# Kernel optimization log

Hardware: AMD Instinct MI355X
Metric: run time of the kernel (lower is better)

The kernel has to match this reference:

```python
import jax, jax.numpy as jnp
import numpy as np

N, DIM, K = 131072, 64, 1024


def setup_inputs() -> dict:
    key = jax.random.key(0)
    kx, ke = jax.random.split(key)
    x = jax.random.normal(kx, (N, DIM), dtype=jnp.float32)
    # codebook buffer, initialized like uniform(-1/K, 1/K) in the original
    scale = 1.0 / K
    embedding = jax.random.uniform(ke, (K, DIM), dtype=jnp.float32, minval=-scale, maxval=scale)
    return {"x": x, "embedding": embedding}


def reference(x, embedding):
    # squared euclidean distances in fp32 (matches compute_distances)
    x32 = x.astype(jnp.float32)
    e32 = embedding.astype(jnp.float32)
    distances = (
        jnp.sum(x32 * x32, axis=1, keepdims=True)
        + jnp.sum(e32 * e32, axis=1)
        - 2.0 * jnp.einsum("nd,kd->nk", x32, e32)
    )
    indices = jnp.argmin(distances, axis=1)          # (N,)
    quantized = embedding[indices]                    # (N, DIM) codebook gather
    # commitment loss: mse(stop_grad(quantized), x)
    commitment_loss = jnp.mean((jax.lax.stop_gradient(quantized) - x) ** 2)
    # straight-through estimator
    quantized_st = x + jax.lax.stop_gradient(quantized - x)
    return quantized_st, indices, commitment_loss
```

## Files before the change

kernel.cpp:

```cpp
#include <hip/hip_runtime.h>
#include <hip/hip_bf16.h>

#define N_ROWS 131072
#define DIM 64
#define K_CODES 1024
#define NTILES 64
#define MARGIN 4e-5f
#define LIST_CAP 65536

typedef short short8 __attribute__((ext_vector_type(8)));
typedef float f32x4 __attribute__((ext_vector_type(4)));

__device__ __forceinline__ unsigned short f2bf(float f) {
    unsigned u = __float_as_uint(f);
    return (unsigned short)((u + 0x7fffu + ((u >> 16) & 1u)) >> 16);
}
__device__ __forceinline__ float bf2f(unsigned short h) {
    return __uint_as_float(((unsigned)h) << 16);
}

__device__ __forceinline__ float np_sq64(const float* __restrict__ v) {
    float xx[DIM];
    #pragma unroll
    for (int d = 0; d < DIM; ++d) xx[d] = v[d] * v[d];
    float r[8];
    #pragma unroll
    for (int j = 0; j < 8; ++j) r[j] = xx[j];
    #pragma unroll
    for (int i = 8; i < DIM; i += 8)
        #pragma unroll
        for (int j = 0; j < 8; ++j) r[j] = r[j] + xx[i + j];
    return ((r[0]+r[1]) + (r[2]+r[3])) + ((r[4]+r[5]) + (r[6]+r[7]));
}

__device__ __forceinline__ float np_dot64(const float* __restrict__ xv,
                                          const float* __restrict__ ek) {
    float a0 = 0.f, a1 = 0.f, a2 = 0.f, a3 = 0.f;
    #pragma unroll
    for (int c = 0; c < DIM; c += 16)
        #pragma unroll
        for (int b = 12; b >= 0; b -= 4) {
            const int d = c + b;
            a0 = a0 + xv[d+0] * ek[d+0];
            a1 = a1 + xv[d+1] * ek[d+1];
            a2 = a2 + xv[d+2] * ek[d+2];
            a3 = a3 + xv[d+3] * ek[d+3];
        }
    return (a0 + a1) + (a2 + a3);
}


__global__ void vq_prep(const float* __restrict__ emb, float* __restrict__ esq,
                        unsigned short* __restrict__ wsB,
                        unsigned int* __restrict__ cnt, float* __restrict__ loss) {
#pragma clang fp contract(off)
    const int t = blockIdx.x * blockDim.x + threadIdx.x;
    if (t == 0) { *cnt = 0u; *loss = 0.f; }
    const int k = t >> 2, c = t & 3;
    if (k >= K_CODES) return;
    const float* e = emb + (size_t)k * DIM;

    if (c == 0) esq[k] = np_sq64(e);

    const int off = (c & 1) * 32, sel = c >> 1;
    unsigned short val[32];
    #pragma unroll
    for (int j = 0; j < 32; ++j) {
        float v = e[off + j];
        unsigned short h = f2bf(v);
        val[j] = sel ? f2bf(v - bf2f(h)) : h;
    }
    const int tile = k >> 4, n = k & 15;
    #pragma unroll
    for (int g = 0; g < 4; ++g) {
        short8 s;
        #pragma unroll
        for (int j = 0; j < 8; ++j) s[j] = (short)val[g*8 + j];
        *reinterpret_cast<short8*>(wsB + ((size_t)((tile*4 + c)*64 + g*16 + n)) * 8) = s;
    }
}

__global__ __launch_bounds__(256, 2) void vq_mfma(const float* __restrict__ x,
        const float* __restrict__ emb, const float* __restrict__ esq,
        const unsigned short* __restrict__ wsB, float* __restrict__ out,
        unsigned int* __restrict__ cnt, unsigned int* __restrict__ list,
        float* __restrict__ loss) {
#pragma clang fp contract(off)
    const int tid = threadIdx.x;
    const int lane = tid & 63;
    const int w = tid >> 6;
    const int g = lane >> 4, res = lane & 15;
    const int rowbase = blockIdx.x * 256 + w * 64;

    auto loadB = [&](short8* Bd, int ct) {
        const unsigned short* bp = wsB + ((size_t)(ct*4)*64 + lane) * 8;
        #pragma unroll
        for (int c = 0; c < 4; ++c)
            Bd[c] = *reinterpret_cast<const short8*>(bp + (size_t)c * 64 * 8);
    };

    short8 B0[4], B1[4], B2[4], B3[4];
    loadB(B0, 0); loadB(B1, 1); loadB(B2, 2); loadB(B3, 3);
    float e0 = esq[res], e1 = esq[16 + res];

    short8 Ah[4][2], Al[4][2];
    #pragma unroll
    for (int rg = 0; rg < 4; ++rg) {
        const float* xr = x + (size_t)(rowbase + rg*16 + res) * DIM;
        #pragma unroll
        for (int h = 0; h < 2; ++h) {
            float4 v0 = *reinterpret_cast<const float4*>(xr + h*32 + g*8);
            float4 v1 = *reinterpret_cast<const float4*>(xr + h*32 + g*8 + 4);
            float xv[8] = {v0.x, v0.y, v0.z, v0.w, v1.x, v1.y, v1.z, v1.w};
            short8 sh, sl;
            #pragma unroll
            for (int j = 0; j < 8; ++j) {
                unsigned short hb = f2bf(xv[j]);
                sh[j] = (short)hb;
                sl[j] = (short)f2bf(xv[j] - bf2f(hb));
            }
            Ah[rg][h] = sh; Al[rg][h] = sl;
        }
    }

    float b1[16], b2[16], b3[16], b4[16];
    const float FINF = __uint_as_float(0x7F800000u);
    #pragma unroll
    for (int s = 0; s < 16; ++s) { b1[s]=FINF; b2[s]=FINF; b3[s]=FINF; b4[s]=FINF; }

    auto MF = [&](f32x4* acc, const short8* B) {
        __builtin_amdgcn_s_setprio(1);
        #pragma unroll
        for (int rg = 0; rg < 4; ++rg) acc[rg] = f32x4{0.f, 0.f, 0.f, 0.f};
        #pragma unroll
        for (int rg = 0; rg < 4; ++rg)
            acc[rg] = __builtin_amdgcn_mfma_f32_16x16x32_bf16(Ah[rg][0], B[0], acc[rg], 0,0,0);
        #pragma unroll
        for (int rg = 0; rg < 4; ++rg)
            acc[rg] = __builtin_amdgcn_mfma_f32_16x16x32_bf16(Ah[rg][1], B[1], acc[rg], 0,0,0);
        #pragma unroll
        for (int rg = 0; rg < 4; ++rg)
            acc[rg] = __builtin_amdgcn_mfma_f32_16x16x32_bf16(Ah[rg][0], B[2], acc[rg], 0,0,0);
        #pragma unroll
        for (int rg = 0; rg < 4; ++rg)
            acc[rg] = __builtin_amdgcn_mfma_f32_16x16x32_bf16(Ah[rg][1], B[3], acc[rg], 0,0,0);
        #pragma unroll
        for (int rg = 0; rg < 4; ++rg)
            acc[rg] = __builtin_amdgcn_mfma_f32_16x16x32_bf16(Al[rg][0], B[0], acc[rg], 0,0,0);
        #pragma unroll
        for (int rg = 0; rg < 4; ++rg)
            acc[rg] = __builtin_amdgcn_mfma_f32_16x16x32_bf16(Al[rg][1], B[1], acc[rg], 0,0,0);
        __builtin_amdgcn_s_setprio(0);
    };

    auto KY = [&](const f32x4* acc, float esqv, int ct) {
        const unsigned kcur = (unsigned)(ct*16 + res);
        #pragma unroll
        for (int rg = 0; rg < 4; ++rg) {
            #pragma unroll
            for (int r = 0; r < 4; ++r) {
                float v = fmaf(-2.0f, acc[rg][r], esqv);
                float key = __uint_as_float((__float_as_uint(v) & 0xFFFFFC00u) | kcur);
                const int s = rg*4 + r;
                float o1 = b1[s], o2 = b2[s], o3 = b3[s];
                b4[s] = __builtin_amdgcn_fmed3f(key, o3, b4[s]);
                b3[s] = __builtin_amdgcn_fmed3f(key, o2, o3);
                b2[s] = __builtin_amdgcn_fmed3f(key, o1, o2);
                b1[s] = fminf(o1, key);
            }
        }
    };

    f32x4 accA[4], accB[4];
    MF(accA, B0);
    for (int p = 0; p < 15; ++p) {
        const int t = 4 * p;
        loadB(B0, t + 4);
        MF(accB, B1);
        KY(accA, e0, t);      e0 = esq[(t + 2) * 16 + res];
        loadB(B1, t + 5);
        MF(accA, B2);
        KY(accB, e1, t + 1);  e1 = esq[(t + 3) * 16 + res];
        loadB(B2, t + 6);
        MF(accB, B3);
        KY(accA, e0, t + 2);  e0 = esq[(t + 4) * 16 + res];
        loadB(B3, t + 7);
        MF(accA, B0);
        KY(accB, e1, t + 3);  e1 = esq[(t + 5) * 16 + res];
    }
    MF(accB, B1);
    KY(accA, e0, 60);  e0 = esq[62 * 16 + res];
    MF(accA, B2);
    KY(accB, e1, 61);  e1 = esq[63 * 16 + res];
    MF(accB, B3);
    KY(accA, e0, 62);
    KY(accB, e1, 63);

    #pragma unroll
    for (int m = 1; m < 16; m <<= 1) {
        #pragma unroll
        for (int s = 0; s < 16; ++s) {
            float oa1 = __shfl_xor(b1[s], m, 64);
            float oa2 = __shfl_xor(b2[s], m, 64);
            float oa3 = __shfl_xor(b3[s], m, 64);
            float oa4 = __shfl_xor(b4[s], m, 64);
            float m1 = fminf(b1[s], oa1);
            float m2 = fminf(fmaxf(b1[s], oa1), fminf(b2[s], oa2));
            float m3 = fminf(fminf(fmaxf(b1[s], oa2), fmaxf(b2[s], oa1)),
                             fminf(b3[s], oa3));
            float m4 = fminf(fminf(fmaxf(b1[s], oa3), fmaxf(b3[s], oa1)),
                             fminf(fmaxf(b2[s], oa2), fminf(b4[s], oa4)));
            b1[s] = m1; b2[s] = m2; b3[s] = m3; b4[s] = m4;
        }
    }

    __shared__ float s_k1[256], s_k2[256], s_k3[256], s_k4[256];
    __shared__ int s_idx[256];
    if (res == 0) {
        #pragma unroll
        for (int s = 0; s < 16; ++s) {
            const int rl = w*64 + (s >> 2)*16 + g*4 + (s & 3);
            s_k1[rl] = b1[s]; s_k2[rl] = b2[s]; s_k3[rl] = b3[s]; s_k4[rl] = b4[s];
        }
    }
    __syncthreads();

    {
        const int row = blockIdx.x * 256 + tid;
        unsigned u1 = __float_as_uint(s_k1[tid]);
        unsigned u2 = __float_as_uint(s_k2[tid]);
        unsigned u3 = __float_as_uint(s_k3[tid]);
        unsigned u4 = __float_as_uint(s_k4[tid]);
        float f1 = __uint_as_float(u1 & 0xFFFFFC00u);
        float f2 = __uint_as_float(u2 & 0xFFFFFC00u);
        float f3 = __uint_as_float(u3 & 0xFFFFFC00u);
        float f4 = __uint_as_float(u4 & 0xFFFFFC00u);
        int idx;
        if (f4 - f1 < MARGIN) {
            unsigned slot = atomicAdd(cnt, 1u);
            if (slot < LIST_CAP) list[slot] = (unsigned)row;
            idx = -1;
        } else if (f2 - f1 < MARGIN) {
            const int nc = (f3 - f1 < MARGIN) ? 3 : 2;
            int cand[3] = {(int)(u1 & 0x3FFu), (int)(u2 & 0x3FFu), (int)(u3 & 0x3FFu)};
            float xv[DIM];
            const float4* xp = reinterpret_cast<const float4*>(x + (size_t)row * DIM);
            #pragma unroll
            for (int q = 0; q < 16; ++q) {
                float4 v = xp[q];
                xv[4*q+0] = v.x; xv[4*q+1] = v.y; xv[4*q+2] = v.z; xv[4*q+3] = v.w;
            }
            float xsq = np_sq64(xv);
            float bd = INFINITY; int bi = 0x7fffffff;
            for (int c = 0; c < nc; ++c) {
                const int k = cand[c];
                float tt = xsq + esq[k];
                float dd = tt - 2.0f * np_dot64(xv, emb + (size_t)k * DIM);
                if (dd < bd || (dd == bd && k < bi)) { bd = dd; bi = k; }
            }
            idx = bi;
        } else {
            idx = (int)(u1 & 0x3FFu);
        }
        s_idx[tid] = idx;
    }
    __syncthreads();

    float lsum = 0.f;
    #pragma unroll
    for (int pass = 0; pass < 2; ++pass) {
        const int rl = (tid >> 1) + pass * 128, half = tid & 1;
        const int row = blockIdx.x * 256 + rl;
        const int idx = s_idx[rl];
        if (idx >= 0) {
            const float* xr = x + (size_t)row * DIM + half*32;
            const float* qr = emb + (size_t)idx * DIM + half*32;
            float* orow = out + (size_t)row * DIM + half*32;
            #pragma unroll
            for (int i = 0; i < 8; ++i) {
                float4 xv = reinterpret_cast<const float4*>(xr)[i];
                float4 qv = reinterpret_cast<const float4*>(qr)[i];
                float df0 = qv.x - xv.x, df1 = qv.y - xv.y;
                float df2 = qv.z - xv.z, df3 = qv.w - xv.w;
                lsum = fmaf(df0, df0, lsum); lsum = fmaf(df1, df1, lsum);
                lsum = fmaf(df2, df2, lsum); lsum = fmaf(df3, df3, lsum);
                float4 o = {xv.x + df0, xv.y + df1, xv.z + df2, xv.w + df3};
                reinterpret_cast<float4*>(orow)[i] = o;
            }
            if (half == 0) out[(size_t)N_ROWS * DIM + row] = (float)idx;
        }
    }
    #pragma unroll
    for (int off = 32; off > 0; off >>= 1) lsum += __shfl_down(lsum, off, 64);
    if (lane == 0) atomicAdd(loss, lsum);
}

__global__ void vq_fixup(const float* __restrict__ x, const float* __restrict__ emb,
                         const float* __restrict__ esq,
                         const unsigned int* __restrict__ cnt,
                         const unsigned int* __restrict__ list,
                         float* __restrict__ out, float* __restrict__ loss) {
#pragma clang fp contract(off)
    const int lane = threadIdx.x & 63;
    const int wid = (blockIdx.x * blockDim.x + threadIdx.x) >> 6;
    const int nw = (256 * 256) >> 6;
    unsigned count = *cnt;
    if (count > LIST_CAP) count = LIST_CAP;
    for (unsigned i = wid; i < count; i += nw) {
        const int row = (int)list[i];
        float xv[DIM];
        const float4* xp = reinterpret_cast<const float4*>(x + (size_t)row * DIM);
        #pragma unroll
        for (int q = 0; q < 16; ++q) {
            float4 v = xp[q];
            xv[4*q+0] = v.x; xv[4*q+1] = v.y; xv[4*q+2] = v.z; xv[4*q+3] = v.w;
        }
        float xsq = np_sq64(xv);
        float best = INFINITY; int bidx = 0x7fffffff;
        for (int t = 0; t < K_CODES / 64; ++t) {
            const int k = lane + t * 64;
            float dot = np_dot64(xv, emb + (size_t)k * DIM);
            float tt = xsq + esq[k];
            float dist = tt - 2.0f * dot;
            if (dist < best) { best = dist; bidx = k; }
        }
        #pragma unroll
        for (int m = 1; m < 64; m <<= 1) {
            float ob = __shfl_xor(best, m, 64);
            int   oi = __shfl_xor(bidx, m, 64);
            if (ob < best || (ob == best && oi < bidx)) { best = ob; bidx = oi; }
        }
        const float xd = x[(size_t)row * DIM + lane];
        const float qd = emb[(size_t)bidx * DIM + lane];
        const float df = qd - xd;
        out[(size_t)row * DIM + lane] = xd + df;
        if (lane == 0) out[(size_t)N_ROWS * DIM + row] = (float)bidx;
        float l2 = df * df;
        #pragma unroll
        for (int off = 32; off > 0; off >>= 1) l2 += __shfl_down(l2, off, 64);
        if (lane == 0) atomicAdd(loss, l2);
    }
}

__global__ void vq_final(const float* __restrict__ loss_acc, float* __restrict__ out_loss) {
    if (threadIdx.x == 0 && blockIdx.x == 0)
        out_loss[0] = loss_acc[0] / (float)((size_t)N_ROWS * DIM);
}

extern "C" void kernel_launch(void* const* d_in, const int* in_sizes, int n_in,
                              void* d_out, int out_size, void* d_ws, size_t ws_size,
                              hipStream_t stream) {
    const float* x   = (const float*)d_in[0];
    const float* emb = (const float*)d_in[1];
    float* out = (float*)d_out;

    unsigned int* cnt  = (unsigned int*)d_ws;
    float* loss        = (float*)d_ws + 1;
    float* esq         = (float*)d_ws + 4;
    unsigned short* wsB = (unsigned short*)((char*)d_ws + 8192);
    unsigned int* list = (unsigned int*)((char*)d_ws + 270336);

    vq_prep<<<dim3(64), dim3(64), 0, stream>>>(emb, esq, wsB, cnt, loss);
    vq_mfma<<<dim3(N_ROWS / 256), dim3(256), 0, stream>>>(x, emb, esq, wsB, out,
                                                          cnt, list, loss);
    vq_fixup<<<dim3(256), dim3(256), 0, stream>>>(x, emb, esq, cnt, list, out, loss);
    vq_final<<<dim3(1), dim3(1), 0, stream>>>(loss, out + (size_t)N_ROWS * DIM + N_ROWS);
}
```

Before: 130.9 us.

## Stage codebook tiles through LDS with async global_load_lds ring buffer

```diff
diff --git a/kernel.cpp b/kernel.cpp
--- a/kernel.cpp
+++ b/kernel.cpp
@@ -10,6 +10,8 @@
 
 typedef short short8 __attribute__((ext_vector_type(8)));
 typedef float f32x4 __attribute__((ext_vector_type(4)));
+typedef const __attribute__((address_space(1))) void* gptr_t;
+typedef __attribute__((address_space(3))) void* lptr_t;
 
 __device__ __forceinline__ unsigned short f2bf(float f) {
     unsigned u = __float_as_uint(f);
@@ -92,16 +94,13 @@
     const int g = lane >> 4, res = lane & 15;
     const int rowbase = blockIdx.x * 256 + w * 64;
 
-    auto loadB = [&](short8* Bd, int ct) {
-        const unsigned short* bp = wsB + ((size_t)(ct*4)*64 + lane) * 8;
-        #pragma unroll
-        for (int c = 0; c < 4; ++c)
-            Bd[c] = *reinterpret_cast<const short8*>(bp + (size_t)c * 64 * 8);
-    };
-
-    short8 B0[4], B1[4], B2[4], B3[4];
-    loadB(B0, 0); loadB(B1, 1); loadB(B2, 2); loadB(B3, 3);
-    float e0 = esq[res], e1 = esq[16 + res];
+    __shared__ __align__(16) unsigned char sB[4][4][4096];
+    __shared__ float s_esq[K_CODES];
+    __shared__ float s_k1[256], s_k2[256], s_k3[256], s_k4[256];
+    __shared__ int s_idx[256];
+
+    for (int i = tid; i < K_CODES; i += 256) s_esq[i] = esq[i];
+    __syncthreads();
 
     short8 Ah[4][2], Al[4][2];
     #pragma unroll
@@ -122,6 +121,20 @@
             Ah[rg][h] = sh; Al[rg][h] = sl;
         }
     }
+
+    const unsigned char* wsBb = (const unsigned char*)wsB;
+    auto stage = [&](int ct, int slot) {
+        const unsigned char* src = wsBb + (size_t)ct * 4096 + lane * 16;
+        #pragma unroll
+        for (int c = 0; c < 4; ++c)
+            __builtin_amdgcn_global_load_lds((gptr_t)(src + c * 1024),
+                                             (lptr_t)&sB[w][slot][c * 1024], 16, 0, 0);
+    };
+    auto readB = [&](short8* Bd, int slot) {
+        #pragma unroll
+        for (int c = 0; c < 4; ++c)
+            Bd[c] = *reinterpret_cast<const short8*>(&sB[w][slot][c * 1024 + lane * 16]);
+    };
 
     float b1[16], b2[16], b3[16], b4[16];
     const float FINF = __uint_as_float(0x7F800000u);
@@ -171,28 +184,41 @@
         }
     };
 
+    stage(0, 0); stage(1, 1); stage(2, 2);
+    float e0 = s_esq[res], e1 = s_esq[16 + res];
+
+    short8 Bc[4];
     f32x4 accA[4], accB[4];
-    MF(accA, B0);
-    for (int p = 0; p < 15; ++p) {
-        const int t = 4 * p;
-        loadB(B0, t + 4);
-        MF(accB, B1);
-        KY(accA, e0, t);      e0 = esq[(t + 2) * 16 + res];
-        loadB(B1, t + 5);
-        MF(accA, B2);
-        KY(accB, e1, t + 1);  e1 = esq[(t + 3) * 16 + res];
-        loadB(B2, t + 6);
-        MF(accB, B3);
-        KY(accA, e0, t + 2);  e0 = esq[(t + 4) * 16 + res];
-        loadB(B3, t + 7);
-        MF(accA, B0);
-        KY(accB, e1, t + 3);  e1 = esq[(t + 5) * 16 + res];
-    }
-    MF(accB, B1);
-    KY(accA, e0, 60);  e0 = esq[62 * 16 + res];
-    MF(accA, B2);
-    KY(accB, e1, 61);  e1 = esq[63 * 16 + res];
-    MF(accB, B3);
+
+    stage(3, 3);
+    asm volatile("s_waitcnt vmcnt(12)" ::: "memory");
+    readB(Bc, 0);
+    MF(accA, Bc);
+
+    for (int p = 0; p < 30; ++p) {
+        const int t = 2 * p + 1;
+        stage(t + 3, (t + 3) & 3);
+        asm volatile("s_waitcnt vmcnt(12)" ::: "memory");
+        readB(Bc, t & 3);
+        MF(accB, Bc);
+        KY(accA, e0, t - 1);  e0 = s_esq[(t + 1) * 16 + res];
+        stage(t + 4, (t + 4) & 3);
+        asm volatile("s_waitcnt vmcnt(12)" ::: "memory");
+        readB(Bc, (t + 1) & 3);
+        MF(accA, Bc);
+        KY(accB, e1, t);      e1 = s_esq[(t + 2) * 16 + res];
+    }
+    asm volatile("s_waitcnt vmcnt(8)" ::: "memory");
+    readB(Bc, 1);
+    MF(accB, Bc);
+    KY(accA, e0, 60);  e0 = s_esq[62 * 16 + res];
+    asm volatile("s_waitcnt vmcnt(4)" ::: "memory");
+    readB(Bc, 2);
+    MF(accA, Bc);
+    KY(accB, e1, 61);  e1 = s_esq[63 * 16 + res];
+    asm volatile("s_waitcnt vmcnt(0)" ::: "memory");
+    readB(Bc, 3);
+    MF(accB, Bc);
     KY(accA, e0, 62);
     KY(accB, e1, 63);
 
@@ -214,8 +240,6 @@
         }
     }
 
-    __shared__ float s_k1[256], s_k2[256], s_k3[256], s_k4[256];
-    __shared__ int s_idx[256];
     if (res == 0) {
         #pragma unroll
         for (int s = 0; s < 16; ++s) {
@@ -254,7 +278,7 @@
             float bd = INFINITY; int bi = 0x7fffffff;
             for (int c = 0; c < nc; ++c) {
                 const int k = cand[c];
-                float tt = xsq + esq[k];
+                float tt = xsq + s_esq[k];
                 float dd = tt - 2.0f * np_dot64(xv, emb + (size_t)k * DIM);
                 if (dd < bd || (dd == bd && k < bi)) { bd = dd; bi = k; }
             }
```

After: 145.1 us. 1.11x slower.
